# Optimization experiments

Hardware: AMD Instinct MI355X
Metric: run time of the kernel (lower is better)

## Reference

```python
import jax, jax.numpy as jnp
import numpy as np

AUDIO_DIM, SEM_DIM, ATTN_DIM = 512, 768, 128


def setup_inputs() -> dict:
    key = jax.random.key(0)
    ks = jax.random.split(key, 12)
    B, T, T_sem = 8, 4096, 1024
    s = lambda d: 1.0 / np.sqrt(d)
    return {
        "x_ct": jax.random.normal(ks[0], (B, AUDIO_DIM, T), jnp.float32),
        "sem_btd": jax.random.normal(ks[1], (B, T_sem, SEM_DIM), jnp.float32),
        "ln_w": jnp.ones((AUDIO_DIM,), jnp.float32),
        "ln_b": jnp.zeros((AUDIO_DIM,), jnp.float32),
        "Wq": jax.random.normal(ks[2], (AUDIO_DIM, ATTN_DIM), jnp.float32) * s(AUDIO_DIM),
        "bq": jnp.zeros((ATTN_DIM,), jnp.float32),
        "Wk": jax.random.normal(ks[3], (SEM_DIM, ATTN_DIM), jnp.float32) * s(SEM_DIM),
        "bk": jnp.zeros((ATTN_DIM,), jnp.float32),
        "Wv": jax.random.normal(ks[4], (SEM_DIM, ATTN_DIM), jnp.float32) * s(SEM_DIM),
        "bv": jnp.zeros((ATTN_DIM,), jnp.float32),
        "Wo": jax.random.normal(ks[5], (ATTN_DIM, AUDIO_DIM), jnp.float32) * s(ATTN_DIM),
        "bo": jnp.zeros((AUDIO_DIM,), jnp.float32),
    }


def _layernorm(x, w, b, eps=1e-5):
    mu = jnp.mean(x, axis=-1, keepdims=True)
    var = jnp.mean(jnp.square(x - mu), axis=-1, keepdims=True)
    return (x - mu) * jax.lax.rsqrt(var + eps) * w + b


def reference(x_ct, sem_btd, ln_w, ln_b, Wq, bq, Wk, bk, Wv, bv, Wo, bo):
    # x_ct: [B, C, T] -> [B, T, C]
    x = jnp.swapaxes(x_ct, 1, 2)
    x = _layernorm(x, ln_w, ln_b)
    Q = x @ Wq + bq                      # [B, T, A]
    K = sem_btd @ Wk + bk                # [B, S, A]
    V = sem_btd @ Wv + bv                # [B, S, A]
    scale = ATTN_DIM ** -0.5
    attn = jnp.einsum("bta,bsa->bts", Q, K) * scale
    attn = jax.nn.softmax(attn, axis=-1)  # dropout: eval mode (identity)
    ctx = jnp.einsum("bts,bsa->bta", attn, V)
    delta = ctx @ Wo + bo                # [B, T, C]
    return jnp.swapaxes(delta, 1, 2)     # [B, C, T]
```

## Files before the change

kernel.cpp:

```cpp
#include <hip/hip_runtime.h>
#include <hip/hip_bf16.h>
#include <math.h>

#define BATCH 8
#define TDIM 4096
#define SDIM 1024
#define CDIM 512
#define DDIM 768
#define ADIM 128

typedef short s8v __attribute__((ext_vector_type(8)));
typedef float f4v __attribute__((ext_vector_type(4)));

__device__ __forceinline__ short f2bf(float f) {
    unsigned u = __float_as_uint(f);
    u += 0x7fffu + ((u >> 16) & 1u);
    return (short)(u >> 16);
}
__device__ __forceinline__ float bf2f(short s) {
    return __uint_as_float(((unsigned)(unsigned short)s) << 16);
}
__device__ __forceinline__ f4v mfma16(s8v a, s8v b, f4v c) {
    return __builtin_amdgcn_mfma_f32_16x16x32_bf16(a, b, c, 0, 0, 0);
}
__device__ __forceinline__ void gl_lds16(const short* g, short* l) {
    __builtin_amdgcn_global_load_lds(
        (const __attribute__((address_space(1))) unsigned int*)g,
        (__attribute__((address_space(3))) unsigned int*)l, 16, 0, 0);
}

__global__ __launch_bounds__(256) void prep_w(
    const float* __restrict__ Wq, const float* __restrict__ Wk,
    const float* __restrict__ Wv, const float* __restrict__ Wo,
    const float* __restrict__ lnw,
    short* __restrict__ WqT, short* __restrict__ WkT,
    short* __restrict__ WvT, short* __restrict__ WoT,
    float* __restrict__ uq)
{
    int gid = blockIdx.x * 256 + threadIdx.x;
    if (blockIdx.x == 0) uq[threadIdx.x] = 0.f;
    {
        int k = gid >> 7, n = gid & 127;
        int idx = (k >> 6) * 8192 + n * 64 + ((((k >> 3) & 7) ^ (n & 7)) * 8) + (k & 7);
        WqT[idx] = f2bf(Wq[gid] * lnw[k]);
    }
    #pragma unroll
    for (int i = 0; i < 2; ++i) {
        int e = gid + i * 65536;
        if (e < 98304) {
            int k = e >> 7, n = e & 127;
            WkT[n * 768 + k] = f2bf(Wk[e]);
            WvT[n * 768 + k] = f2bf(Wv[e]);
        }
    }
    {
        int k = gid >> 9, c = gid & 511;
        WoT[c * 128 + k] = f2bf(Wo[gid]);
    }
}

__global__ __launch_bounds__(256) void prep_uv(
    const float* __restrict__ Wq, const float* __restrict__ lnw,
    const float* __restrict__ lnb,
    float* __restrict__ uq, float* __restrict__ vq)
{
    __shared__ float r1[128], r2[128];
    const int a = threadIdx.x & 127, h = threadIdx.x >> 7;
    const int c = blockIdx.x * 2 + h;
    float wv = Wq[c * 128 + a];
    float s1 = bf2f(f2bf(lnw[c] * wv));
    float s2 = lnb[c] * wv;
    if (h) { r1[a] = s1; r2[a] = s2; }
    __syncthreads();
    if (!h) {
        atomicAdd(&uq[a], s1 + r1[a]);
        atomicAdd(&vq[a], s2 + r2[a]);
    }
}

__global__ __launch_bounds__(256) void kv_proj(
    const float* __restrict__ sem,
    const short* __restrict__ WkT, const float* __restrict__ bk,
    const short* __restrict__ WvT, const float* __restrict__ bv,
    short* __restrict__ Kb, short* __restrict__ Vb)
{
    __shared__ __align__(16) short sA[32 * 40];
    __shared__ __align__(16) short sW[2][128 * 40];
    const int tid = threadIdx.x, lane = tid & 63, wave = tid >> 6;
    const int ln15 = lane & 15, q = lane >> 4, kq = q * 8;
    const int r0 = blockIdx.x * 32;
    const int b = r0 >> 10, sbase = r0 & 1023;
    const int kv = wave >> 1;
    const int mh = wave & 1;
    const int m  = mh * 16 + ln15;

    f4v acc[8];
    #pragma unroll
    for (int j = 0; j < 8; ++j) acc[j] = (f4v)0.0f;

    const int srow = tid >> 3;
    const int sk4  = (tid & 7) * 4;

    for (int kc = 0; kc < DDIM / 32; ++kc) {
        __syncthreads();
        {
            float4 f = *(const float4*)&sem[(size_t)(r0 + srow) * DDIM + kc * 32 + sk4];
            uint2 pk;
            pk.x = (unsigned short)f2bf(f.x) | ((unsigned)(unsigned short)f2bf(f.y) << 16);
            pk.y = (unsigned short)f2bf(f.z) | ((unsigned)(unsigned short)f2bf(f.w) << 16);
            *(uint2*)&sA[srow * 40 + sk4] = pk;
        }
        #pragma unroll
        for (int i = 0; i < 2; ++i) {
            int idx8 = i * 256 + tid;
            int n = idx8 >> 2, k8 = (idx8 & 3) * 8;
            *(s8v*)&sW[0][n * 40 + k8] = *(const s8v*)&WkT[(size_t)n * 768 + kc * 32 + k8];
            *(s8v*)&sW[1][n * 40 + k8] = *(const s8v*)&WvT[(size_t)n * 768 + kc * 32 + k8];
        }
        __syncthreads();
        s8v a = *(const s8v*)&sA[m * 40 + kq];
        #pragma unroll
        for (int j = 0; j < 8; ++j) {
            s8v bb = *(const s8v*)&sW[kv][(j * 16 + ln15) * 40 + kq];
            acc[j] = mfma16(a, bb, acc[j]);
        }
    }
    const int s_in_b = sbase + mh * 16 + q * 4;
    if (kv == 0) {
        #pragma unroll
        for (int j = 0; j < 8; ++j) {
            int col = j * 16 + ln15;
            float bias = bk[col];
            #pragma unroll
            for (int r = 0; r < 4; ++r)
                Kb[((size_t)b * SDIM + s_in_b + r) * ADIM + col] = f2bf(acc[j][r] + bias);
        }
    } else {
        #pragma unroll
        for (int j = 0; j < 8; ++j) {
            int col = j * 16 + ln15;
            float bias = bv[col];
            uint2 pk;
            pk.x = (unsigned short)f2bf(acc[j][0] + bias) | ((unsigned)(unsigned short)f2bf(acc[j][1] + bias) << 16);
            pk.y = (unsigned short)f2bf(acc[j][2] + bias) | ((unsigned)(unsigned short)f2bf(acc[j][3] + bias) << 16);
            *(uint2*)&Vb[((size_t)b * ADIM + col) * SDIM + s_in_b] = pk;
        }
    }
}

__global__ __launch_bounds__(512) void ln_q(
    const float* __restrict__ x,
    const short* __restrict__ WqI, const float* __restrict__ uq,
    const float* __restrict__ vq, const float* __restrict__ bq,
    short* __restrict__ Qb)
{
    __shared__ __align__(16) short sX[2][128 * 72];
    __shared__ __align__(16) short sW[2][64 * 128];
    __shared__ __align__(16) float redw[8][32][4][2];
    const int tid = threadIdx.x, lane = tid & 63, wave = tid >> 6;
    const int ln15 = lane & 15, q = lane >> 4, kq = q * 8;
    const int b = blockIdx.x >> 5;
    const int t0 = (blockIdx.x & 31) * 128;
    const float* xb = x + (size_t)b * CDIM * TDIM + t0;

    const int l5 = lane >> 5;
    const int tq = (lane & 31) * 4;
    const int cw = wave * 2 + l5;

    float ps1[4] = {0.f,0.f,0.f,0.f}, ps2[4] = {0.f,0.f,0.f,0.f};
    const int m = wave * 16 + ln15;
    const int swzm = m & 7;
    f4v acc[8];
    #pragma unroll
    for (int j = 0; j < 8; ++j) acc[j] = (f4v)0.0f;

    float4 xv[4];

#define PROC_X(BUF) do {                                                      \
    _Pragma("unroll")                                                         \
    for (int i = 0; i < 4; ++i) {                                             \
        float4 v = xv[i];                                                     \
        ps1[0] += v.x; ps2[0] += v.x * v.x;                                   \
        ps1[1] += v.y; ps2[1] += v.y * v.y;                                   \
        ps1[2] += v.z; ps2[2] += v.z * v.z;                                   \
        ps1[3] += v.w; ps2[3] += v.w * v.w;                                   \
        float o0 = __shfl_xor(v.x, 32); float o1 = __shfl_xor(v.y, 32);       \
        float o2 = __shfl_xor(v.z, 32); float o3 = __shfl_xor(v.w, 32);       \
        const int ccE = i * 16 + wave * 2;                                    \
        unsigned wA, wB; int tA, tB;                                          \
        if (l5 == 0) {                                                        \
            tA = tq; tB = tq + 1;                                             \
            wA = (unsigned short)f2bf(v.x) | ((unsigned)(unsigned short)f2bf(o0) << 16); \
            wB = (unsigned short)f2bf(v.y) | ((unsigned)(unsigned short)f2bf(o1) << 16); \
        } else {                                                              \
            tA = tq + 2; tB = tq + 3;                                         \
            wA = (unsigned short)f2bf(o2) | ((unsigned)(unsigned short)f2bf(v.z) << 16); \
            wB = (unsigned short)f2bf(o3) | ((unsigned)(unsigned short)f2bf(v.w) << 16); \
        }                                                                     \
        *(unsigned*)&sX[BUF][tA * 72 + (((ccE >> 3) ^ (tA & 7)) * 8) + (ccE & 7)] = wA; \
        *(unsigned*)&sX[BUF][tB * 72 + (((ccE >> 3) ^ (tB & 7)) * 8) + (ccE & 7)] = wB; \
    }                                                                         \
} while (0)

    #pragma unroll
    for (int i = 0; i < 4; ++i)
        xv[i] = *(const float4*)&xb[(size_t)(i * 16 + cw) * TDIM + tq];
    #pragma unroll
    for (int i = 0; i < 2; ++i) {
        int gi = i * 512 + wave * 64;
        gl_lds16(&WqI[(size_t)(gi + lane) * 8], &sW[0][gi * 8]);
    }
    PROC_X(0);
    __syncthreads();

    for (int kc = 0; kc < 8; ++kc) {
        const int cur = kc & 1;
        if (kc < 7) {
            const float* xc = xb + (size_t)(kc + 1) * 64 * TDIM;
            #pragma unroll
            for (int i = 0; i < 4; ++i)
                xv[i] = *(const float4*)&xc[(size_t)(i * 16 + cw) * TDIM + tq];
            const short* wch = WqI + (size_t)(kc + 1) * 8192;
            #pragma unroll
            for (int i = 0; i < 2; ++i) {
                int gi = i * 512 + wave * 64;
                gl_lds16(&wch[(size_t)(gi + lane) * 8], &sW[cur ^ 1][gi * 8]);
            }
        }
        #pragma unroll
        for (int kk = 0; kk < 2; ++kk) {
            s8v a = *(const s8v*)&sX[cur][m * 72 + (((kk * 4 + q) ^ swzm) * 8)];
            #pragma unroll
            for (int j = 0; j < 8; ++j) {
                int n = j * 16 + ln15;
                s8v bb = *(const s8v*)&sW[cur][n * 64 + (((kk * 4 + q) ^ (n & 7)) * 8)];
                acc[j] = mfma16(a, bb, acc[j]);
            }
        }
        if (kc < 7) PROC_X(cur ^ 1);
        __syncthreads();
    }

    #pragma unroll
    for (int jj = 0; jj < 4; ++jj) {
        ps1[jj] += __shfl_xor(ps1[jj], 32);
        ps2[jj] += __shfl_xor(ps2[jj], 32);
    }
    if (lane < 32) {
        #pragma unroll
        for (int jj = 0; jj < 4; ++jj) {
            redw[wave][lane][jj][0] = ps1[jj];
            redw[wave][lane][jj][1] = ps2[jj];
        }
    }
    __syncthreads();

    float u4[8], v4[8];
    #pragma unroll
    for (int j = 0; j < 8; ++j) {
        int col = j * 16 + ln15;
        u4[j] = uq[col]; v4[j] = vq[col] + bq[col];
    }
    const float scale = 0.08838834764831845f;
    const int quad = wave * 4 + q;
    #pragma unroll
    for (int r = 0; r < 4; ++r) {
        float s1 = 0.f, s2 = 0.f;
        #pragma unroll
        for (int w = 0; w < 8; ++w) {
            float2 p = *(const float2*)&redw[w][quad][r][0];
            s1 += p.x; s2 += p.y;
        }
        float mu = s1 * (1.f / 512.f);
        float var = s2 * (1.f / 512.f) - mu * mu;
        float rs = rsqrtf(var + 1e-5f);
        int t = t0 + wave * 16 + q * 4 + r;
        #pragma unroll
        for (int j = 0; j < 8; ++j) {
            float qv = (rs * (acc[j][r] - mu * u4[j]) + v4[j]) * scale;
            Qb[((size_t)b * TDIM + t) * ADIM + (j * 16 + ln15)] = f2bf(qv);
        }
    }
#undef PROC_X
}

__global__ __launch_bounds__(256) void attn(
    const short* __restrict__ Qb, const short* __restrict__ Kb,
    const short* __restrict__ Vb, short* __restrict__ Cx)
{
    __shared__ __align__(16) short sK [2][64 * 128];
    __shared__ __align__(16) short sVT[2][128 * 64];
    __shared__ __align__(16) short sP [64 * 64];
    const int tid = threadIdx.x, lane = tid & 63, wave = tid >> 6;
    const int ln15 = lane & 15, q = lane >> 4, kq = q * 8;
    const int b = blockIdx.x >> 6;
    const int t0 = (blockIdx.x & 63) * 64;
    const int m = wave * 16 + ln15;

    const int krow = tid >> 4, kkb = tid & 15;
    const int varow = tid >> 3, vkb = tid & 7;

    s8v qf[4];
    {
        const short* qp = Qb + ((size_t)b * TDIM + t0 + m) * ADIM + kq;
        #pragma unroll
        for (int kc = 0; kc < 4; ++kc) qf[kc] = *(const s8v*)(qp + kc * 32);
    }
    s8v ones;
    #pragma unroll
    for (int j = 0; j < 8; ++j) ones[j] = (short)0x3F80;

    f4v accO[8]; f4v accL = (f4v)0.0f;
    #pragma unroll
    for (int j = 0; j < 8; ++j) accO[j] = (f4v)0.0f;

    const short* Kbase = Kb + (size_t)b * SDIM * ADIM;
    const short* Vbase = Vb + (size_t)b * ADIM * SDIM;
    s8v rk[4], rv[4];

    #pragma unroll
    for (int i = 0; i < 4; ++i) {
        rk[i] = *(const s8v*)(Kbase + (size_t)(i * 16 + krow) * ADIM + kkb * 8);
        rv[i] = *(const s8v*)(Vbase + (size_t)(i * 32 + varow) * SDIM + vkb * 8);
    }
    #pragma unroll
    for (int i = 0; i < 4; ++i) {
        int r = i * 16 + krow;
        *(s8v*)&sK[0][r * 128 + ((kkb ^ (r & 15)) * 8)] = rk[i];
        int a = i * 32 + varow;
        *(s8v*)&sVT[0][a * 64 + ((vkb ^ (a & 7)) * 8)] = rv[i];
    }
    __syncthreads();

    for (int sc = 0; sc < SDIM / 64; ++sc) {
        const int cur = sc & 1;
        if (sc < 15) {
            const int s0n = (sc + 1) * 64;
            #pragma unroll
            for (int i = 0; i < 4; ++i) {
                rk[i] = *(const s8v*)(Kbase + (size_t)(s0n + i * 16 + krow) * ADIM + kkb * 8);
                rv[i] = *(const s8v*)(Vbase + (size_t)(i * 32 + varow) * SDIM + s0n + vkb * 8);
            }
        }
        #pragma unroll
        for (int j = 0; j < 4; ++j) {
            f4v sacc = (f4v)0.0f;
            const int row = j * 16 + ln15;
            #pragma unroll
            for (int kc = 0; kc < 4; ++kc) {
                s8v bb = *(const s8v*)&sK[cur][row * 128 + (((kc * 4 + q) ^ (row & 15)) * 8)];
                sacc = mfma16(qf[kc], bb, sacc);
            }
            #pragma unroll
            for (int r = 0; r < 4; ++r) {
                float ev = __expf(sacc[r]);
                int prow = wave * 16 + q * 4 + r;
                int pcol = j * 16 + ln15;
                sP[prow * 64 + (((pcol >> 3) ^ (prow & 7)) * 8) + (pcol & 7)] = f2bf(ev);
            }
        }
        #pragma unroll
        for (int kc = 0; kc < 2; ++kc) {
            s8v pa = *(const s8v*)&sP[m * 64 + (((kc * 4 + q) ^ (m & 7)) * 8)];
            accL = mfma16(pa, ones, accL);
            #pragma unroll
            for (int j = 0; j < 8; ++j) {
                int a = j * 16 + ln15;
                s8v bb = *(const s8v*)&sVT[cur][a * 64 + (((kc * 4 + q) ^ (a & 7)) * 8)];
                accO[j] = mfma16(pa, bb, accO[j]);
            }
        }
        if (sc < 15) {
            #pragma unroll
            for (int i = 0; i < 4; ++i) {
                int r = i * 16 + krow;
                *(s8v*)&sK[cur ^ 1][r * 128 + ((kkb ^ (r & 15)) * 8)] = rk[i];
                int a = i * 32 + varow;
                *(s8v*)&sVT[cur ^ 1][a * 64 + ((vkb ^ (a & 7)) * 8)] = rv[i];
            }
        }
        __syncthreads();
    }
    #pragma unroll
    for (int r = 0; r < 4; ++r) {
        float rinv = 1.0f / accL[r];
        int t = t0 + wave * 16 + q * 4 + r;
        #pragma unroll
        for (int j = 0; j < 8; ++j) {
            int col = j * 16 + ln15;
            Cx[((size_t)b * TDIM + t) * ADIM + col] = f2bf(accO[j][r] * rinv);
        }
    }
}

__global__ __launch_bounds__(256) void out_proj(
    const short* __restrict__ Cx, const short* __restrict__ WoT,
    const float* __restrict__ bo, float* __restrict__ out)
{
    __shared__ __align__(16) short sCtx[64 * 136];
    __shared__ __align__(16) char  buf[128 * 136 * 2];
    short* sWoT = (short*)buf;
    float* outT = (float*)buf;
    const int tid = threadIdx.x, lane = tid & 63, wave = tid >> 6;
    const int ln15 = lane & 15, q = lane >> 4, kq = q * 8;
    const int b = blockIdx.x >> 8;
    const int rem = blockIdx.x & 255;
    const int t0 = (rem & 63) * 64;
    const int c0 = (rem >> 6) * 128;

    #pragma unroll
    for (int i = 0; i < 4; ++i) {
        int idx8 = i * 256 + tid;
        int row = idx8 >> 4, a8 = (idx8 & 15) * 8;
        *(s8v*)&sCtx[row * 136 + a8] = *(const s8v*)&Cx[((size_t)b * TDIM + t0 + row) * ADIM + a8];
    }
    #pragma unroll
    for (int i = 0; i < 8; ++i) {
        int idx8 = i * 256 + tid;
        int n = idx8 >> 4, k8 = (idx8 & 15) * 8;
        *(s8v*)&sWoT[n * 136 + k8] = *(const s8v*)&WoT[(size_t)(c0 + n) * ADIM + k8];
    }
    __syncthreads();
    f4v acc[8];
    #pragma unroll
    for (int j = 0; j < 8; ++j) acc[j] = (f4v)0.0f;
    const int m = wave * 16 + ln15;
    #pragma unroll
    for (int kc = 0; kc < 4; ++kc) {
        s8v a = *(const s8v*)&sCtx[m * 136 + kc * 32 + kq];
        #pragma unroll
        for (int j = 0; j < 8; ++j) {
            s8v bb = *(const s8v*)&sWoT[(j * 16 + ln15) * 136 + kc * 32 + kq];
            acc[j] = mfma16(a, bb, acc[j]);
        }
    }
    __syncthreads();
    #pragma unroll
    for (int j = 0; j < 8; ++j) {
        int cl = j * 16 + ln15;
        float bias = bo[c0 + cl];
        #pragma unroll
        for (int r = 0; r < 4; ++r) {
            int tl = wave * 16 + q * 4 + r;
            outT[cl * 68 + tl] = acc[j][r] + bias;
        }
    }
    __syncthreads();
    #pragma unroll
    for (int i = 0; i < 8; ++i) {
        int idx4 = i * 256 + tid;
        int c = idx4 >> 4, t4 = (idx4 & 15) * 4;
        float4 v = *(const float4*)&outT[c * 68 + t4];
        *(float4*)&out[((size_t)b * CDIM + c0 + c) * TDIM + t0 + t4] = v;
    }
}

extern "C" void kernel_launch(void* const* d_in, const int* in_sizes, int n_in,
                              void* d_out, int out_size, void* d_ws, size_t ws_size,
                              hipStream_t stream) {
    const float* x   = (const float*)d_in[0];
    const float* sem = (const float*)d_in[1];
    const float* lnw = (const float*)d_in[2];
    const float* lnb = (const float*)d_in[3];
    const float* Wq  = (const float*)d_in[4];
    const float* bq  = (const float*)d_in[5];
    const float* Wk  = (const float*)d_in[6];
    const float* bk  = (const float*)d_in[7];
    const float* Wv  = (const float*)d_in[8];
    const float* bv  = (const float*)d_in[9];
    const float* Wo  = (const float*)d_in[10];
    const float* bo  = (const float*)d_in[11];
    float* out = (float*)d_out;

    short* ws  = (short*)d_ws;
    short* Qb  = ws;
    short* Kb  = Qb  + (size_t)BATCH * TDIM * ADIM;
    short* Vb  = Kb  + (size_t)BATCH * SDIM * ADIM;
    short* Cx  = Vb  + (size_t)BATCH * SDIM * ADIM;
    short* WqT = Cx  + (size_t)BATCH * TDIM * ADIM;
    short* WkT = WqT + 128 * 512;
    short* WvT = WkT + 128 * 768;
    short* WoT = WvT + 128 * 768;
    float* uq  = (float*)(WoT + 512 * 128);
    float* vq  = uq + 128;

    hipLaunchKernelGGL(prep_w,  dim3(256),  dim3(256), 0, stream,
                       Wq, Wk, Wv, Wo, lnw, WqT, WkT, WvT, WoT, uq);
    hipLaunchKernelGGL(prep_uv, dim3(256),  dim3(256), 0, stream, Wq, lnw, lnb, uq, vq);
    hipLaunchKernelGGL(kv_proj, dim3(256),  dim3(256), 0, stream, sem, WkT, bk, WvT, bv, Kb, Vb);
    hipLaunchKernelGGL(ln_q,    dim3(256),  dim3(512), 0, stream, x, WqT, uq, vq, bq, Qb);
    hipLaunchKernelGGL(attn,    dim3(512),  dim3(256), 0, stream, Qb, Kb, Vb, Cx);
    hipLaunchKernelGGL(out_proj,dim3(2048), dim3(256), 0, stream, Cx, WoT, bo, out);
}
```

Before: 241.5 us.

## Halve ln_q time tile to 64 rows and split output columns across waves

```diff
diff --git a/kernel.cpp b/kernel.cpp
--- a/kernel.cpp
+++ b/kernel.cpp
@@ -148,63 +148,66 @@
     }
 }
 
-__global__ __launch_bounds__(512) void ln_q(
+__global__ __launch_bounds__(512, 4) void ln_q(
     const float* __restrict__ x,
     const short* __restrict__ WqI, const float* __restrict__ uq,
     const float* __restrict__ vq, const float* __restrict__ bq,
     short* __restrict__ Qb)
 {
-    __shared__ __align__(16) short sX[2][128 * 72];
+    __shared__ __align__(16) short sX[2][64 * 72];
     __shared__ __align__(16) short sW[2][64 * 128];
-    __shared__ __align__(16) float redw[8][32][4][2];
+    __shared__ __align__(16) float redw[8][16][4][2];
     const int tid = threadIdx.x, lane = tid & 63, wave = tid >> 6;
     const int ln15 = lane & 15, q = lane >> 4, kq = q * 8;
-    const int b = blockIdx.x >> 5;
-    const int t0 = (blockIdx.x & 31) * 128;
+    const int b = blockIdx.x >> 6;
+    const int t0 = (blockIdx.x & 63) * 64;
     const float* xb = x + (size_t)b * CDIM * TDIM + t0;
 
-    const int l5 = lane >> 5;
-    const int tq = (lane & 31) * 4;
-    const int cw = wave * 2 + l5;
+    const int rg = lane >> 4;
+    const int g  = rg & 1;
+    const int L  = lane & 15;
+    const int t4 = L * 4;
+    const int crow = wave * 4 + rg;
 
     float ps1[4] = {0.f,0.f,0.f,0.f}, ps2[4] = {0.f,0.f,0.f,0.f};
-    const int m = wave * 16 + ln15;
-    const int swzm = m & 7;
-    f4v acc[8];
-    #pragma unroll
-    for (int j = 0; j < 8; ++j) acc[j] = (f4v)0.0f;
-
-    float4 xv[4];
+    const int wr = wave & 3, wc = wave >> 2;
+    const int m = wr * 16 + ln15;
+    const int swzm = (m >> 2) & 7;
+    f4v acc[4];
+    #pragma unroll
+    for (int j = 0; j < 4; ++j) acc[j] = (f4v)0.0f;
+
+    float4 xv[2];
 
 #define PROC_X(BUF) do {                                                      \
     _Pragma("unroll")                                                         \
-    for (int i = 0; i < 4; ++i) {                                             \
+    for (int i = 0; i < 2; ++i) {                                             \
         float4 v = xv[i];                                                     \
         ps1[0] += v.x; ps2[0] += v.x * v.x;                                   \
         ps1[1] += v.y; ps2[1] += v.y * v.y;                                   \
         ps1[2] += v.z; ps2[2] += v.z * v.z;                                   \
         ps1[3] += v.w; ps2[3] += v.w * v.w;                                   \
-        float o0 = __shfl_xor(v.x, 32); float o1 = __shfl_xor(v.y, 32);       \
-        float o2 = __shfl_xor(v.z, 32); float o3 = __shfl_xor(v.w, 32);       \
-        const int ccE = i * 16 + wave * 2;                                    \
+        float o0 = __shfl_xor(v.x, 16); float o1 = __shfl_xor(v.y, 16);       \
+        float o2 = __shfl_xor(v.z, 16); float o3 = __shfl_xor(v.w, 16);       \
+        const int c   = crow + i * 32;                                        \
+        const int cdw = c & ~1;                                               \
         unsigned wA, wB; int tA, tB;                                          \
-        if (l5 == 0) {                                                        \
-            tA = tq; tB = tq + 1;                                             \
+        if (g == 0) {                                                         \
+            tA = t4; tB = t4 + 1;                                             \
             wA = (unsigned short)f2bf(v.x) | ((unsigned)(unsigned short)f2bf(o0) << 16); \
             wB = (unsigned short)f2bf(v.y) | ((unsigned)(unsigned short)f2bf(o1) << 16); \
         } else {                                                              \
-            tA = tq + 2; tB = tq + 3;                                         \
+            tA = t4 + 2; tB = t4 + 3;                                         \
             wA = (unsigned short)f2bf(o2) | ((unsigned)(unsigned short)f2bf(v.z) << 16); \
             wB = (unsigned short)f2bf(o3) | ((unsigned)(unsigned short)f2bf(v.w) << 16); \
         }                                                                     \
-        *(unsigned*)&sX[BUF][tA * 72 + (((ccE >> 3) ^ (tA & 7)) * 8) + (ccE & 7)] = wA; \
-        *(unsigned*)&sX[BUF][tB * 72 + (((ccE >> 3) ^ (tB & 7)) * 8) + (ccE & 7)] = wB; \
+        *(unsigned*)&sX[BUF][tA * 72 + (((cdw >> 3) ^ ((tA >> 2) & 7)) * 8) + (cdw & 7)] = wA; \
+        *(unsigned*)&sX[BUF][tB * 72 + (((cdw >> 3) ^ ((tB >> 2) & 7)) * 8) + (cdw & 7)] = wB; \
     }                                                                         \
 } while (0)
 
-    #pragma unroll
-    for (int i = 0; i < 4; ++i)
-        xv[i] = *(const float4*)&xb[(size_t)(i * 16 + cw) * TDIM + tq];
+    xv[0] = *(const float4*)&xb[(size_t)crow * TDIM + t4];
+    xv[1] = *(const float4*)&xb[(size_t)(crow + 32) * TDIM + t4];
     #pragma unroll
     for (int i = 0; i < 2; ++i) {
         int gi = i * 512 + wave * 64;
@@ -217,9 +220,8 @@
         const int cur = kc & 1;
         if (kc < 7) {
             const float* xc = xb + (size_t)(kc + 1) * 64 * TDIM;
-            #pragma unroll
-            for (int i = 0; i < 4; ++i)
-                xv[i] = *(const float4*)&xc[(size_t)(i * 16 + cw) * TDIM + tq];
+            xv[0] = *(const float4*)&xc[(size_t)crow * TDIM + t4];
+            xv[1] = *(const float4*)&xc[(size_t)(crow + 32) * TDIM + t4];
             const short* wch = WqI + (size_t)(kc + 1) * 8192;
             #pragma unroll
             for (int i = 0; i < 2; ++i) {
@@ -231,8 +233,8 @@
         for (int kk = 0; kk < 2; ++kk) {
             s8v a = *(const s8v*)&sX[cur][m * 72 + (((kk * 4 + q) ^ swzm) * 8)];
             #pragma unroll
-            for (int j = 0; j < 8; ++j) {
-                int n = j * 16 + ln15;
+            for (int j = 0; j < 4; ++j) {
+                int n = wc * 64 + j * 16 + ln15;
                 s8v bb = *(const s8v*)&sW[cur][n * 64 + (((kk * 4 + q) ^ (n & 7)) * 8)];
                 acc[j] = mfma16(a, bb, acc[j]);
             }
@@ -242,27 +244,30 @@
     }
 
     #pragma unroll
-    for (int jj = 0; jj < 4; ++jj) {
-        ps1[jj] += __shfl_xor(ps1[jj], 32);
-        ps2[jj] += __shfl_xor(ps2[jj], 32);
-    }
-    if (lane < 32) {
+    for (int mk = 16; mk <= 32; mk <<= 1) {
         #pragma unroll
         for (int jj = 0; jj < 4; ++jj) {
-            redw[wave][lane][jj][0] = ps1[jj];
-            redw[wave][lane][jj][1] = ps2[jj];
-        }
-    }
-    __syncthreads();
-
-    float u4[8], v4[8];
-    #pragma unroll
-    for (int j = 0; j < 8; ++j) {
-        int col = j * 16 + ln15;
+            ps1[jj] += __shfl_xor(ps1[jj], mk);
+            ps2[jj] += __shfl_xor(ps2[jj], mk);
+        }
+    }
+    if (lane < 16) {
+        #pragma unroll
+        for (int jj = 0; jj < 4; ++jj) {
+            redw[wave][L][jj][0] = ps1[jj];
+            redw[wave][L][jj][1] = ps2[jj];
+        }
+    }
+    __syncthreads();
+
+    float u4[4], v4[4];
+    #pragma unroll
+    for (int j = 0; j < 4; ++j) {
+        int col = wc * 64 + j * 16 + ln15;
         u4[j] = uq[col]; v4[j] = vq[col] + bq[col];
     }
     const float scale = 0.08838834764831845f;
-    const int quad = wave * 4 + q;
+    const int quad = wr * 4 + q;
     #pragma unroll
     for (int r = 0; r < 4; ++r) {
         float s1 = 0.f, s2 = 0.f;
@@ -274,11 +279,11 @@
         float mu = s1 * (1.f / 512.f);
         float var = s2 * (1.f / 512.f) - mu * mu;
         float rs = rsqrtf(var + 1e-5f);
-        int t = t0 + wave * 16 + q * 4 + r;
-        #pragma unroll
-        for (int j = 0; j < 8; ++j) {
+        int t = t0 + wr * 16 + q * 4 + r;
+        #pragma unroll
+        for (int j = 0; j < 4; ++j) {
             float qv = (rs * (acc[j][r] - mu * u4[j]) + v4[j]) * scale;
-            Qb[((size_t)b * TDIM + t) * ADIM + (j * 16 + ln15)] = f2bf(qv);
+            Qb[((size_t)b * TDIM + t) * ADIM + (wc * 64 + j * 16 + ln15)] = f2bf(qv);
         }
     }
 #undef PROC_X
@@ -488,7 +493,7 @@
                        Wq, Wk, Wv, Wo, lnw, WqT, WkT, WvT, WoT, uq);
     hipLaunchKernelGGL(prep_uv, dim3(256),  dim3(256), 0, stream, Wq, lnw, lnb, uq, vq);
     hipLaunchKernelGGL(kv_proj, dim3(256),  dim3(256), 0, stream, sem, WkT, bk, WvT, bv, Kb, Vb);
-    hipLaunchKernelGGL(ln_q,    dim3(256),  dim3(512), 0, stream, x, WqT, uq, vq, bq, Qb);
+    hipLaunchKernelGGL(ln_q,    dim3(512),  dim3(512), 0, stream, x, WqT, uq, vq, bq, Qb);
     hipLaunchKernelGGL(attn,    dim3(512),  dim3(256), 0, stream, Qb, Kb, Vb, Cx);
     hipLaunchKernelGGL(out_proj,dim3(2048), dim3(256), 0, stream, Cx, WoT, bo, out);
 }
```

Result: faster. 234.1 us (-3.0%).
